# Performance work log

Hardware: AMD Instinct MI355X
Metric: run time of the kernel (lower is better)

## Reference

```python
import jax, jax.numpy as jnp
import numpy as np

S = 8192
D = 512

def setup_inputs() -> dict:
    key = jax.random.key(0)
    k1, k2, k3, k4 = jax.random.split(key, 4)
    token_encodings = jax.random.normal(k1, (S, D), dtype=jnp.float32)
    # causal mask: True where attention is disallowed (strictly upper triangular)
    mask = jnp.triu(jnp.ones((S, S), dtype=bool), k=1)
    W_q = jax.random.normal(k2, (D, D), dtype=jnp.float32) * (1.0 / np.sqrt(D))
    W_k = jax.random.normal(k3, (D, D), dtype=jnp.float32) * (1.0 / np.sqrt(D))
    W_v = jax.random.normal(k4, (D, D), dtype=jnp.float32) * (1.0 / np.sqrt(D))
    return {"token_encodings": token_encodings, "mask": mask, "W_q": W_q, "W_k": W_k, "W_v": W_v}

def reference(token_encodings, mask, W_q, W_k, W_v):
    # nn.Linear(bias=False): y = x @ W^T
    q = token_encodings @ W_q.T  # [S, D]
    k = token_encodings @ W_k.T  # [S, D]
    v = token_encodings @ W_v.T  # [S, D]
    scale = jnp.asarray(k.shape[1], dtype=q.dtype) ** 0.5
    sims = (q @ k.T) / scale  # [S, S]
    sims = jnp.where(mask, jnp.asarray(-1e9, dtype=sims.dtype), sims)
    attn = jax.nn.softmax(sims, axis=1)
    return attn @ v  # [S, D]
```

## Files before the change

kernel.cpp:

```cpp
#include <hip/hip_runtime.h>
#include <stdint.h>

typedef _Float16 f16;
typedef _Float16 f16x8 __attribute__((ext_vector_type(8)));
typedef _Float16 f16x4 __attribute__((ext_vector_type(4)));
typedef float f32x4 __attribute__((ext_vector_type(4)));

#define S_TOK 8192
#define DDIM  512
#define L2E   1.44269504088896340736f
#define QSCALE 0.04419417382415922f
#define NSLOT 320
#define GTOT  8320

__device__ __forceinline__ void gload_lds16(const void* g, void* l) {
  __builtin_amdgcn_global_load_lds((const __attribute__((address_space(1))) void*)g,
                                   (__attribute__((address_space(3))) void*)l, 16, 0, 0);
}

template <int C>
__device__ __forceinline__ float fdpp(float x) {
  return __builtin_bit_cast(float,
      __builtin_amdgcn_update_dpp(0, __builtin_bit_cast(int, x), C, 0xF, 0xF, true));
}
__device__ __forceinline__ float rowmax16(float x) {
  x = fmaxf(x, fdpp<0xB1>(x));
  x = fmaxf(x, fdpp<0x4E>(x));
  x = fmaxf(x, fdpp<0x141>(x));
  x = fmaxf(x, fdpp<0x140>(x));
  return x;
}
__device__ __forceinline__ float rowsum16(float x) {
  x += fdpp<0xB1>(x);
  x += fdpp<0x4E>(x);
  x += fdpp<0x141>(x);
  x += fdpp<0x140>(x);
  return x;
}

__global__ __launch_bounds__(256) void k_convert(
    const float* __restrict__ X, const float* __restrict__ Wq,
    const float* __restrict__ Wk, const float* __restrict__ Wv,
    f16* __restrict__ Xh, f16* __restrict__ Wh, int* __restrict__ tp) {
  const int SD = S_TOK * DDIM;
  const int DD = DDIM * DDIM;
  int gi = blockIdx.x * 256 + threadIdx.x;
  if (gi < NSLOT) tp[gi] = -1;
  int i4 = gi * 4;
  if (i4 < SD) {
    f32x4 v = *(const f32x4*)(X + i4);
    f16x4 h = {(f16)v[0], (f16)v[1], (f16)v[2], (f16)v[3]};
    *(f16x4*)(Xh + i4) = h;
  } else {
    int j = i4 - SD;
    int mat = j >> 18;
    const float* src = (mat == 0) ? Wq : (mat == 1 ? Wk : Wv);
    f32x4 v = *(const f32x4*)(src + (j & (DD - 1)));
    f16x4 h = {(f16)v[0], (f16)v[1], (f16)v[2], (f16)v[3]};
    *(f16x4*)(Wh + j) = h;
  }
}

__global__ __launch_bounds__(256) void k_proj(
    const f16* __restrict__ Xh, const f16* __restrict__ Wh,
    f16* __restrict__ Qh, f16* __restrict__ Kh, f16* __restrict__ VB) {
  __shared__ __align__(16) char Al[128 * 128];
  __shared__ __align__(16) char Bl[128 * 128];
  const int tid = threadIdx.x;
  const int w = tid >> 6, lane = tid & 63;
  const int m0 = blockIdx.x * 128;
  const int n0 = blockIdx.y * 128;
  const int wr = (w >> 1) * 64;
  const int wc = (w & 1) * 64;

  f32x4 acc[4][4];
#pragma unroll
  for (int i = 0; i < 4; ++i)
#pragma unroll
    for (int j = 0; j < 4; ++j) acc[i][j] = (f32x4){0.f, 0.f, 0.f, 0.f};

  const char* Xb = (const char*)Xh;
  const char* Wb = (const char*)Wh;

  for (int kb = 0; kb < DDIM; kb += 64) {
    __syncthreads();
#pragma unroll
    for (int i = 0; i < 4; ++i) {
      int ch = w * 4 + i;
      int srow = lane >> 3;
      int scol = ((lane & 7) * 16) ^ (srow << 4);
      gload_lds16(Xb + (size_t)(m0 + ch * 8 + srow) * 1024 + kb * 2 + scol, Al + ch * 1024);
      gload_lds16(Wb + (size_t)(n0 + ch * 8 + srow) * 1024 + kb * 2 + scol, Bl + ch * 1024);
    }
    __syncthreads();
#pragma unroll
    for (int ks = 0; ks < 2; ++ks) {
      f16x8 a[4], b[4];
#pragma unroll
      for (int mf = 0; mf < 4; ++mf) {
        int row = wr + mf * 16 + (lane & 15);
        int col = (ks * 64 + ((lane >> 4) * 16)) ^ ((row & 7) << 4);
        a[mf] = *(const f16x8*)(Al + row * 128 + col);
      }
#pragma unroll
      for (int nf = 0; nf < 4; ++nf) {
        int row = wc + nf * 16 + (lane & 15);
        int col = (ks * 64 + ((lane >> 4) * 16)) ^ ((row & 7) << 4);
        b[nf] = *(const f16x8*)(Bl + row * 128 + col);
      }
#pragma unroll
      for (int mf = 0; mf < 4; ++mf)
#pragma unroll
        for (int nf = 0; nf < 4; ++nf)
          acc[mf][nf] = __builtin_amdgcn_mfma_f32_16x16x32_f16(a[mf], b[nf], acc[mf][nf], 0, 0, 0);
    }
  }
  int mat = n0 >> 9;
  int nbase = n0 & 511;
  if (mat == 2) {
#pragma unroll
    for (int mf = 0; mf < 4; ++mf) {
      int R0 = m0 + wr + mf * 16 + (lane >> 4) * 4;
      int K = R0 >> 5;
      int lhi = ((R0 >> 3) & 3) * 16;
      int j0 = R0 & 7;
#pragma unroll
      for (int nf = 0; nf < 4; ++nf) {
        int col = nbase + wc + nf * 16 + (lane & 15);
        f16x4 h = {(f16)acc[mf][nf][0], (f16)acc[mf][nf][1],
                   (f16)acc[mf][nf][2], (f16)acc[mf][nf][3]};
        *(f16x4*)((char*)VB + (size_t)(K * 32 + (col >> 4)) * 1024 +
                  (lhi + (col & 15)) * 16 + j0 * 2) = h;
      }
    }
  } else {
    f16* dst = (mat == 0) ? Qh : Kh;
    float scale = (mat == 0) ? QSCALE : 1.0f;
#pragma unroll
    for (int mf = 0; mf < 4; ++mf)
#pragma unroll
      for (int nf = 0; nf < 4; ++nf)
#pragma unroll
        for (int r = 0; r < 4; ++r) {
          int row = m0 + wr + mf * 16 + (lane >> 4) * 4 + r;
          int col = nbase + wc + nf * 16 + (lane & 15);
          dst[(size_t)row * DDIM + col] = (f16)(acc[mf][nf][r] * scale);
        }
  }
}

__global__ __launch_bounds__(512, 2) void k_flash(
    const f16* __restrict__ Qh, const f16* __restrict__ Kh,
    const f16* __restrict__ VBg, f16* __restrict__ Opart,
    float* __restrict__ Mpart, float* __restrict__ Lpart,
    int* __restrict__ TilePart) {
  __shared__ __align__(16) char Kl[2][32768];
  __shared__ __align__(16) char Vl[2][32768];
  __shared__ __align__(16) char Pl[8][2][1152];

  const int tid = threadIdx.x;
  const int w = tid >> 6, lane = tid & 63;
  const int l15 = lane & 15, l4 = lane >> 4;

  int bid = blockIdx.x;
  int b = (bid & 7) * 32 + (bid >> 3);
  int g  = (GTOT * b) >> 8;
  int g1 = (GTOT * (b + 1)) >> 8;
  int t = 0;
  while (2 * (t + 1) * (t + 2) <= g) ++t;

  const char* Kb = (const char*)Kh;
  const char* Vb = (const char*)VBg;

#define STAGEKV(KB, BI) do {                                                   \
    _Pragma("unroll")                                                          \
    for (int i_ = 0; i_ < 4; ++i_) {                                           \
      int row_ = w * 4 + i_;                                                   \
      int scol_ = (lane * 16) ^ ((row_ & 7) << 4);                             \
      gload_lds16(Kb + (size_t)((KB) + row_) * 1024 + scol_, Kl[BI] + row_ * 1024); \
    }                                                                          \
    const char* vs_ = Vb + (size_t)(KB) * 1024;                                \
    _Pragma("unroll")                                                          \
    for (int i_ = 0; i_ < 4; ++i_) {                                           \
      int ch_ = w * 4 + i_;                                                    \
      gload_lds16(vs_ + ch_ * 1024 + lane * 16, Vl[BI] + ch_ * 1024);          \
    } } while (0)

#define SOFTMAX(KB, Pdst) do {                                                 \
    float p0[4], p1[4], mx[4];                                                 \
    int qrb = q0 + w * 16 + l4 * 4;                                            \
    int kc = (KB) + l15;                                                       \
    _Pragma("unroll")                                                          \
    for (int r = 0; r < 4; ++r) {                                              \
      int qr = qrb + r;                                                        \
      float x0 = (kc      <= qr) ? s0[r] : -3.0e38f;                           \
      float x1 = (kc + 16 <= qr) ? s1[r] : -3.0e38f;                           \
      p0[r] = x0; p1[r] = x1;                                                  \
      mx[r] = rowmax16(fmaxf(x0, x1));                                         \
    }                                                                          \
    bool need = (mx[0] > mreg[0] + 8.f) || (mx[1] > mreg[1] + 8.f) ||          \
                (mx[2] > mreg[2] + 8.f) || (mx[3] > mreg[3] + 8.f);            \
    if (__any(need)) {                                                         \
      float alpha[4];                                                          \
      _Pragma("unroll")                                                        \
      for (int r = 0; r < 4; ++r) {                                            \
        float mn = fmaxf(mreg[r], mx[r]);                                      \
        alpha[r] = exp2f((mreg[r] - mn) * L2E);                                \
        lreg[r] *= alpha[r];                                                   \
        mreg[r] = mn;                                                          \
      }                                                                        \
      _Pragma("unroll")                                                        \
      for (int nf = 0; nf < 32; ++nf) {                                        \
        acc[nf][0] *= alpha[0];                                                \
        acc[nf][1] *= alpha[1];                                                \
        acc[nf][2] *= alpha[2];                                                \
        acc[nf][3] *= alpha[3];                                                \
      }                                                                        \
    }                                                                          \
    _Pragma("unroll")                                                          \
    for (int r = 0; r < 4; ++r) {                                              \
      int qr = qrb + r;                                                        \
      p0[r] = (kc      <= qr) ? exp2f((p0[r] - mreg[r]) * L2E) : 0.f;          \
      p1[r] = (kc + 16 <= qr) ? exp2f((p1[r] - mreg[r]) * L2E) : 0.f;          \
    }                                                                          \
    _Pragma("unroll")                                                          \
    for (int r = 0; r < 4; ++r) {                                              \
      int row = l4 * 4 + r;                                                    \
      *(f16*)((Pdst) + row * 72 + l15 * 2)      = (f16)p0[r];                  \
      *(f16*)((Pdst) + row * 72 + 32 + l15 * 2) = (f16)p1[r];                  \
    }                                                                          \
    _Pragma("unroll")                                                          \
    for (int r = 0; r < 4; ++r)                                                \
      lreg[r] += rowsum16(p0[r] + p1[r]);                                      \
  } while (0)

#define QKT(BUF) do {                                                          \
    s0 = (f32x4){0.f, 0.f, 0.f, 0.f};                                          \
    s1 = (f32x4){0.f, 0.f, 0.f, 0.f};                                          \
    _Pragma("unroll")                                                          \
    for (int ks = 0; ks < 16; ++ks) {                                          \
      int off = ks * 64 + l4 * 16;                                             \
      f16x8 kf0 = *(const f16x8*)((BUF) + l15 * 1024 + (off ^ ((l15 & 7) << 4))); \
      s0 = __builtin_amdgcn_mfma_f32_16x16x32_f16(qf[ks], kf0, s0, 0, 0, 0);   \
      f16x8 kf1 = *(const f16x8*)((BUF) + (16 + l15) * 1024 + (off ^ ((l15 & 7) << 4))); \
      s1 = __builtin_amdgcn_mfma_f32_16x16x32_f16(qf[ks], kf1, s1, 0, 0, 0);   \
    } } while (0)

  char* Pw = (char*)Pl + (size_t)w * 2304;

  while (g < g1) {
    int Ct  = 2 * t * (t + 1);
    int Ct1 = 2 * (t + 1) * (t + 2);
    int gend = min(g1, Ct1);
    int n = gend - g;
    int kb0 = (g - Ct) * 32;
    int q0 = t * 128;
    int slot = b + t;

    f16x8 qf[16];
    {
      const f16* qp = Qh + (size_t)(q0 + w * 16 + l15) * DDIM + l4 * 8;
#pragma unroll
      for (int ks = 0; ks < 16; ++ks) qf[ks] = *(const f16x8*)(qp + ks * 32);
    }
    f32x4 acc[32];
#pragma unroll
    for (int i = 0; i < 32; ++i) acc[i] = (f32x4){0.f, 0.f, 0.f, 0.f};
    float mreg[4], lreg[4];
#pragma unroll
    for (int r = 0; r < 4; ++r) { mreg[r] = -3.0e38f; lreg[r] = 0.f; }
    f32x4 s0, s1;

    STAGEKV(kb0, 0);
    asm volatile("s_waitcnt vmcnt(0)" ::: "memory");
    __builtin_amdgcn_s_barrier();
    QKT(Kl[0]);
    if (n > 1) STAGEKV(kb0 + 32, 1);
    SOFTMAX(kb0, Pw);
    if (n > 1) asm volatile("s_waitcnt vmcnt(0)" ::: "memory");
    __builtin_amdgcn_s_barrier();

    for (int it = 1; it < n; ++it) {
      const char* KlB = Kl[it & 1];
      const char* VlB = Vl[(it - 1) & 1];
      const char* Pp  = Pw + ((it - 1) & 1) * 1152;
      f16x8 pa = *(const f16x8*)(Pp + l15 * 72 + l4 * 16);
      s0 = (f32x4){0.f, 0.f, 0.f, 0.f};
      s1 = (f32x4){0.f, 0.f, 0.f, 0.f};
      __builtin_amdgcn_s_setprio(1);
#pragma unroll
      for (int ks = 0; ks < 16; ++ks) {
        int off = ks * 64 + l4 * 16;
        f16x8 kf0 = *(const f16x8*)(KlB + l15 * 1024 + (off ^ ((l15 & 7) << 4)));
        s0 = __builtin_amdgcn_mfma_f32_16x16x32_f16(qf[ks], kf0, s0, 0, 0, 0);
        f16x8 vb0 = *(const f16x8*)(VlB + (2 * ks) * 1024 + lane * 16);
        acc[2 * ks] = __builtin_amdgcn_mfma_f32_16x16x32_f16(pa, vb0, acc[2 * ks], 0, 0, 0);
        f16x8 kf1 = *(const f16x8*)(KlB + (16 + l15) * 1024 + (off ^ ((l15 & 7) << 4)));
        s1 = __builtin_amdgcn_mfma_f32_16x16x32_f16(qf[ks], kf1, s1, 0, 0, 0);
        f16x8 vb1 = *(const f16x8*)(VlB + (2 * ks + 1) * 1024 + lane * 16);
        acc[2 * ks + 1] = __builtin_amdgcn_mfma_f32_16x16x32_f16(pa, vb1, acc[2 * ks + 1], 0, 0, 0);
      }
      __builtin_amdgcn_s_setprio(0);
      __builtin_amdgcn_s_barrier();

      if (it + 1 < n) STAGEKV(kb0 + (it + 1) * 32, (it + 1) & 1);
      SOFTMAX(kb0 + it * 32, Pw + (it & 1) * 1152);
      if (it + 1 < n) asm volatile("s_waitcnt vmcnt(0)" ::: "memory");
      __builtin_amdgcn_s_barrier();
    }

    {
      const char* VlB = Vl[(n - 1) & 1];
      const char* Pp  = Pw + ((n - 1) & 1) * 1152;
      f16x8 pa = *(const f16x8*)(Pp + l15 * 72 + l4 * 16);
      __builtin_amdgcn_s_setprio(1);
#pragma unroll
      for (int nf = 0; nf < 32; ++nf) {
        f16x8 vb = *(const f16x8*)(VlB + nf * 1024 + lane * 16);
        acc[nf] = __builtin_amdgcn_mfma_f32_16x16x32_f16(pa, vb, acc[nf], 0, 0, 0);
      }
      __builtin_amdgcn_s_setprio(0);
    }
    __builtin_amdgcn_s_barrier();

    {
      float inv[4];
#pragma unroll
      for (int r = 0; r < 4; ++r) inv[r] = (lreg[r] > 0.f) ? 1.f / lreg[r] : 0.f;
      f16* op = Opart + (size_t)slot * (128 * 512);
      int rowb = w * 16 + l4 * 4;
#pragma unroll
      for (int nf = 0; nf < 32; ++nf) {
        int col = nf * 16 + l15;
#pragma unroll
        for (int r = 0; r < 4; ++r)
          op[(size_t)(rowb + r) * 512 + col] = (f16)(acc[nf][r] * inv[r]);
      }
      if (l15 == 0) {
#pragma unroll
        for (int r = 0; r < 4; ++r) {
          Mpart[slot * 128 + rowb + r] = mreg[r];
          Lpart[slot * 128 + rowb + r] = lreg[r];
        }
      }
      if (tid == 0) TilePart[slot] = t;
    }
    g = gend;
    ++t;
  }
#undef STAGEKV
#undef SOFTMAX
#undef QKT
}

__global__ __launch_bounds__(256) void k_reduce(
    const f16* __restrict__ Opart, const float* __restrict__ Mpart,
    const float* __restrict__ Lpart, const int* __restrict__ TilePart,
    float* __restrict__ out) {
  __shared__ int tp[NSLOT];
  __shared__ int sl[16];
  __shared__ int scnt;
  int tid = threadIdx.x;
  int t = blockIdx.x >> 2, rg = blockIdx.x & 3;
  for (int s = tid; s < NSLOT; s += 256) tp[s] = TilePart[s];
  __syncthreads();
  if (tid == 0) {
    int c = 0;
    for (int s = 0; s < NSLOT; ++s)
      if (tp[s] == t && c < 16) sl[c++] = s;
    scnt = c;
  }
  __syncthreads();
  int cnt = scnt;
  int rowIn = rg * 32 + (tid >> 3);
  int row = t * 128 + rowIn;
  int col0 = (tid & 7) * 64;

  float M = -3.0e38f;
  for (int i = 0; i < cnt; ++i) M = fmaxf(M, Mpart[sl[i] * 128 + rowIn]);
  float a[64];
#pragma unroll
  for (int j = 0; j < 64; ++j) a[j] = 0.f;
  float denom = 0.f;
  for (int i = 0; i < cnt; ++i) {
    int s = sl[i];
    float m = Mpart[s * 128 + rowIn];
    float l = Lpart[s * 128 + rowIn];
    float wgt = exp2f((m - M) * L2E) * l;
    denom += wgt;
    const f16* op = Opart + (size_t)s * 65536 + rowIn * 512 + col0;
#pragma unroll
    for (int v = 0; v < 8; ++v) {
      f16x8 x = *(const f16x8*)(op + v * 8);
#pragma unroll
      for (int j = 0; j < 8; ++j) a[v * 8 + j] += wgt * (float)x[j];
    }
  }
  float inv = (denom > 0.f) ? 1.f / denom : 0.f;
  float* o = out + (size_t)row * 512 + col0;
#pragma unroll
  for (int j = 0; j < 64; ++j) o[j] = a[j] * inv;
}

extern "C" void kernel_launch(void* const* d_in, const int* in_sizes, int n_in,
                              void* d_out, int out_size, void* d_ws, size_t ws_size,
                              hipStream_t stream) {
  const float* X  = (const float*)d_in[0];
  const float* Wq = (const float*)d_in[2];
  const float* Wk = (const float*)d_in[3];
  const float* Wv = (const float*)d_in[4];
  float* out = (float*)d_out;

  char* ws = (char*)d_ws;
  f16*   Opart = (f16*)(ws);
  float* Mpart = (float*)(ws + (40u << 20));
  float* Lpart = (float*)(ws + (41u << 20));
  int*   TileP = (int*)(ws + (42u << 20));
  f16* Qh = (f16*)(ws + (43u << 20));
  f16* Kh = (f16*)(ws + (51u << 20));
  f16* VB = (f16*)(ws + (59u << 20));
  f16* Xh = (f16*)(ws + (67u << 20));
  f16* Wh = (f16*)(ws + (75u << 20));

  k_convert<<<4864, 256, 0, stream>>>(X, Wq, Wk, Wv, Xh, Wh, TileP);
  dim3 gp(64, 12);
  k_proj<<<gp, 256, 0, stream>>>(Xh, Wh, Qh, Kh, VB);
  k_flash<<<256, 512, 0, stream>>>(Qh, Kh, VB, Opart, Mpart, Lpart, TileP);
  k_reduce<<<256, 256, 0, stream>>>(Opart, Mpart, Lpart, TileP, out);
}
```

Before: 250.3 us.

## Reorder attention loop to one barrier per iteration with earlier KV prefetch

Restructures the main flash-attention loop so each iteration runs P·V on the previous block, waits for the prefetched K/V, passes one barrier, then issues the next prefetch and runs QK^T plus softmax. This removes the second barrier per iteration and issues the first prefetch before the initial QK^T, giving the global loads more time in flight. It also adds setprio around the QK^T MFMAs. In exchange, the interleaving of QK and PV MFMAs within one loop is lost, which may reduce MFMA/LDS overlap inside a wave.

```diff
diff --git a/kernel.cpp b/kernel.cpp
--- a/kernel.cpp
+++ b/kernel.cpp
@@ -237,6 +237,7 @@
 #define QKT(BUF) do {                                                          \
     s0 = (f32x4){0.f, 0.f, 0.f, 0.f};                                          \
     s1 = (f32x4){0.f, 0.f, 0.f, 0.f};                                          \
+    __builtin_amdgcn_s_setprio(1);                                             \
     _Pragma("unroll")                                                          \
     for (int ks = 0; ks < 16; ++ks) {                                          \
       int off = ks * 64 + l4 * 16;                                             \
@@ -244,7 +245,20 @@
       s0 = __builtin_amdgcn_mfma_f32_16x16x32_f16(qf[ks], kf0, s0, 0, 0, 0);   \
       f16x8 kf1 = *(const f16x8*)((BUF) + (16 + l15) * 1024 + (off ^ ((l15 & 7) << 4))); \
       s1 = __builtin_amdgcn_mfma_f32_16x16x32_f16(qf[ks], kf1, s1, 0, 0, 0);   \
-    } } while (0)
+    }                                                                          \
+    __builtin_amdgcn_s_setprio(0); } while (0)
+
+#define PV(BI) do {                                                            \
+    const char* VlB_ = Vl[BI];                                                 \
+    const char* Pp_ = Pw + (BI) * 1152;                                        \
+    f16x8 pa_ = *(const f16x8*)(Pp_ + l15 * 72 + l4 * 16);                     \
+    __builtin_amdgcn_s_setprio(1);                                             \
+    _Pragma("unroll")                                                          \
+    for (int nf = 0; nf < 32; ++nf) {                                          \
+      f16x8 vb_ = *(const f16x8*)(VlB_ + nf * 1024 + lane * 16);               \
+      acc[nf] = __builtin_amdgcn_mfma_f32_16x16x32_f16(pa_, vb_, acc[nf], 0, 0, 0); \
+    }                                                                          \
+    __builtin_amdgcn_s_setprio(0); } while (0)
 
   char* Pw = (char*)Pl + (size_t)w * 2304;
 
@@ -274,53 +288,20 @@
     STAGEKV(kb0, 0);
     asm volatile("s_waitcnt vmcnt(0)" ::: "memory");
     __builtin_amdgcn_s_barrier();
+    if (n > 1) STAGEKV(kb0 + 32, 1);
     QKT(Kl[0]);
-    if (n > 1) STAGEKV(kb0 + 32, 1);
     SOFTMAX(kb0, Pw);
-    if (n > 1) asm volatile("s_waitcnt vmcnt(0)" ::: "memory");
-    __builtin_amdgcn_s_barrier();
 
     for (int it = 1; it < n; ++it) {
-      const char* KlB = Kl[it & 1];
-      const char* VlB = Vl[(it - 1) & 1];
-      const char* Pp  = Pw + ((it - 1) & 1) * 1152;
-      f16x8 pa = *(const f16x8*)(Pp + l15 * 72 + l4 * 16);
-      s0 = (f32x4){0.f, 0.f, 0.f, 0.f};
-      s1 = (f32x4){0.f, 0.f, 0.f, 0.f};
-      __builtin_amdgcn_s_setprio(1);
-#pragma unroll
-      for (int ks = 0; ks < 16; ++ks) {
-        int off = ks * 64 + l4 * 16;
-        f16x8 kf0 = *(const f16x8*)(KlB + l15 * 1024 + (off ^ ((l15 & 7) << 4)));
-        s0 = __builtin_amdgcn_mfma_f32_16x16x32_f16(qf[ks], kf0, s0, 0, 0, 0);
-        f16x8 vb0 = *(const f16x8*)(VlB + (2 * ks) * 1024 + lane * 16);
-        acc[2 * ks] = __builtin_amdgcn_mfma_f32_16x16x32_f16(pa, vb0, acc[2 * ks], 0, 0, 0);
-        f16x8 kf1 = *(const f16x8*)(KlB + (16 + l15) * 1024 + (off ^ ((l15 & 7) << 4)));
-        s1 = __builtin_amdgcn_mfma_f32_16x16x32_f16(qf[ks], kf1, s1, 0, 0, 0);
-        f16x8 vb1 = *(const f16x8*)(VlB + (2 * ks + 1) * 1024 + lane * 16);
-        acc[2 * ks + 1] = __builtin_amdgcn_mfma_f32_16x16x32_f16(pa, vb1, acc[2 * ks + 1], 0, 0, 0);
-      }
-      __builtin_amdgcn_s_setprio(0);
+      PV((it - 1) & 1);
+      asm volatile("s_waitcnt vmcnt(0)" ::: "memory");
       __builtin_amdgcn_s_barrier();
-
       if (it + 1 < n) STAGEKV(kb0 + (it + 1) * 32, (it + 1) & 1);
+      QKT(Kl[it & 1]);
       SOFTMAX(kb0 + it * 32, Pw + (it & 1) * 1152);
-      if (it + 1 < n) asm volatile("s_waitcnt vmcnt(0)" ::: "memory");
-      __builtin_amdgcn_s_barrier();
-    }
-
-    {
-      const char* VlB = Vl[(n - 1) & 1];
-      const char* Pp  = Pw + ((n - 1) & 1) * 1152;
-      f16x8 pa = *(const f16x8*)(Pp + l15 * 72 + l4 * 16);
-      __builtin_amdgcn_s_setprio(1);
-#pragma unroll
-      for (int nf = 0; nf < 32; ++nf) {
-        f16x8 vb = *(const f16x8*)(VlB + nf * 1024 + lane * 16);
-        acc[nf] = __builtin_amdgcn_mfma_f32_16x16x32_f16(pa, vb, acc[nf], 0, 0, 0);
-      }
-      __builtin_amdgcn_s_setprio(0);
-    }
+    }
+
+    PV((n - 1) & 1);
     __builtin_amdgcn_s_barrier();
 
     {
@@ -351,6 +332,7 @@
 #undef STAGEKV
 #undef SOFTMAX
 #undef QKT
+#undef PV
 }
 
 __global__ __launch_bounds__(256) void k_reduce(
```

Measured after the change: 242.6 us. 1.03x faster.
